# Optimization experiments

Measured on AMD Instinct MI355X. Metric: run time of the kernel, lower is better.

The kernel has to match this reference:

```python
import jax, jax.numpy as jnp
import numpy as np

N_NODES = 100000

def setup_inputs() -> dict:
    key = jax.random.key(0)
    k1, k2, k3, k4 = jax.random.split(key, 4)
    feat = jax.random.normal(k1, (N_NODES, 128), dtype=jnp.float32)
    weight = jax.random.normal(k2, (128, 64), dtype=jnp.float32) * 0.05
    src = jax.random.randint(k3, (600000,), 0, N_NODES, dtype=jnp.int64)
    dst = jax.random.randint(k4, (600000,), 0, N_NODES, dtype=jnp.int64)
    return {"feat": feat, "weight": weight, "src": src, "dst": dst}

def reference(feat, weight, src, dst):
    n = feat.shape[0]
    ones = jnp.ones(src.shape[0], dtype=jnp.float32)
    # out-degree of source nodes (edges leave src), in-degree of dst nodes
    out_deg = jnp.clip(jax.ops.segment_sum(ones, src, num_segments=n), 1.0)
    in_deg = jnp.clip(jax.ops.segment_sum(ones, dst, num_segments=n), 1.0)
    norm_src = (out_deg ** -0.5)[:, None]   # [N,1]
    norm_dst = (in_deg ** -0.5)[:, None]    # [N,1]
    # in_feats (128) > out_feats (64): project first, then aggregate
    h = jnp.matmul(feat, weight) * norm_src              # [N, 64]
    msgs = h[src]                                        # [E, 64] gather
    rst = jax.ops.segment_sum(msgs, dst, num_segments=n)  # [N, 64] scatter-sum
    rst = rst * norm_dst
    return rst
```

## Files before the change

kernel.cpp:

```cpp
#include <hip/hip_runtime.h>
#include <hip/hip_fp16.h>

#define IN_F 128
#define OUT_F 64
#define NB    256
#define BSH   9
#define CAP   3840
#define CHUNK 2048
#define KPF  136
#define KPW  144

using short8  = __attribute__((ext_vector_type(8))) short;
using float4v = __attribute__((ext_vector_type(4))) float;

static __device__ inline unsigned short f2bf(float x) {
    union { float f; unsigned u; } v; v.f = x;
    unsigned r = (v.u + 0x7fffu + ((v.u >> 16) & 1u)) >> 16;
    return (unsigned short)r;
}

__global__ __launch_bounds__(256) void bin_kernel(
    const int* __restrict__ src, const int* __restrict__ dst,
    int* __restrict__ gcur_d, int* __restrict__ gcur_s,
    unsigned* __restrict__ bkt_d, unsigned short* __restrict__ bkt_s, int E)
{
    __shared__ int hd[NB], hs[NB], based[NB], bases[NB];
    const int tid = threadIdx.x;
    const int e0  = blockIdx.x * CHUNK;

    hd[tid] = 0; hs[tid] = 0;
    __syncthreads();

    int sv[8], dv[8];
    #pragma unroll
    for (int j = 0; j < 8; ++j) {
        int i = e0 + j * 256 + tid;
        if (i < E) { sv[j] = src[i]; dv[j] = dst[i]; }
        else       { sv[j] = -1;     dv[j] = -1; }
    }
    #pragma unroll
    for (int j = 0; j < 8; ++j) {
        if (dv[j] >= 0) {
            atomicAdd(&hd[dv[j] >> BSH], 1);
            atomicAdd(&hs[sv[j] >> BSH], 1);
        }
    }
    __syncthreads();

    int cd = hd[tid], cs = hs[tid];
    based[tid] = cd ? atomicAdd(&gcur_d[tid], cd) : 0;
    bases[tid] = cs ? atomicAdd(&gcur_s[tid], cs) : 0;
    hd[tid] = 0; hs[tid] = 0;
    __syncthreads();

    #pragma unroll
    for (int j = 0; j < 8; ++j) {
        if (dv[j] >= 0) {
            int bd = dv[j] >> BSH;
            int pd = atomicAdd(&hd[bd], 1) + based[bd];
            if (pd < CAP)
                bkt_d[(size_t)bd * CAP + pd] =
                    (unsigned)sv[j] | ((unsigned)(dv[j] & 511) << 17);
            int bs = sv[j] >> BSH;
            int ps = atomicAdd(&hs[bs], 1) + bases[bs];
            if (ps < CAP) bkt_s[(size_t)bs * CAP + ps] = (unsigned short)(sv[j] & 511);
        }
    }
}

__global__ __launch_bounds__(256) void csr_kernel(
    const unsigned* __restrict__ bkt_d, const unsigned short* __restrict__ bkt_s,
    const int* __restrict__ gcur_d, const int* __restrict__ gcur_s,
    int2* __restrict__ off_deg, int* __restrict__ ebuf, int* __restrict__ outdeg, int n)
{
    __shared__ int hist[512], curs[512], hist_s[512], sc[256];
    const int b = blockIdx.x, tid = threadIdx.x;
    const int cnt   = min(gcur_d[b], CAP);
    const int cnt_s = min(gcur_s[b], CAP);

    hist[tid] = 0; hist[tid + 256] = 0;
    hist_s[tid] = 0; hist_s[tid + 256] = 0;
    __syncthreads();

    unsigned rec[15];
    int nrec = 0;
    for (int i = tid; i < cnt; i += 256) {
        unsigned e = bkt_d[(size_t)b * CAP + i];
        rec[nrec++] = e;
        atomicAdd(&hist[e >> 17], 1);
    }
    for (int i = tid; i < cnt_s; i += 256)
        atomicAdd(&hist_s[bkt_s[(size_t)b * CAP + i]], 1);
    __syncthreads();

    int a0 = hist[2 * tid], a1 = hist[2 * tid + 1];
    int psum = a0 + a1;
    sc[tid] = psum; __syncthreads();
    for (int o = 1; o < 256; o <<= 1) {
        int t = (tid >= o) ? sc[tid - o] : 0;
        __syncthreads();
        sc[tid] += t;
        __syncthreads();
    }
    int excl = sc[tid] - psum;
    curs[2 * tid]     = excl;
    curs[2 * tid + 1] = excl + a0;
    off_deg[b * 512 + 2 * tid]     = make_int2(b * CAP + excl,      a0);
    off_deg[b * 512 + 2 * tid + 1] = make_int2(b * CAP + excl + a0, a1);
    __syncthreads();

    for (int j = 0; j < nrec; ++j) {
        unsigned e = rec[j];
        int p = atomicAdd(&curs[e >> 17], 1);
        if (p < CAP) ebuf[b * CAP + p] = (int)(e & 0x1FFFFu);
    }

    int node = b * 512 + tid;
    if (node < n) outdeg[node] = hist_s[tid];
    node += 256;
    if (node < n) outdeg[node] = hist_s[tid + 256];
}

__global__ __launch_bounds__(256) void gemm_norm_kernel(
    const float* __restrict__ feat,
    const float* __restrict__ W,
    const int*   __restrict__ outdeg,
    __half* __restrict__ h,
    int n)
{
    __shared__ unsigned short Fh[128 * KPF];
    __shared__ unsigned short Wt[64 * KPW];

    const int tid  = threadIdx.x;
    const int row0 = blockIdx.x * 128;

    {
        const float4* W4 = (const float4*)W;
        #pragma unroll
        for (int it = 0; it < 8; ++it) {
            int i4 = it * 256 + tid;
            int k  = i4 >> 4;
            int c4 = (i4 & 15) * 4;
            float4 wv = W4[i4];
            Wt[(c4 + 0) * KPW + k] = f2bf(wv.x);
            Wt[(c4 + 1) * KPW + k] = f2bf(wv.y);
            Wt[(c4 + 2) * KPW + k] = f2bf(wv.z);
            Wt[(c4 + 3) * KPW + k] = f2bf(wv.w);
        }
    }
    {
        const float4* F4 = (const float4*)feat;
        #pragma unroll
        for (int it = 0; it < 16; ++it) {
            int i4 = it * 256 + tid;
            int r  = i4 >> 5;
            int c4 = (i4 & 31) * 4;
            int gr = row0 + r; if (gr >= n) gr = n - 1;
            float4 v = F4[(long)gr * 32 + (i4 & 31)];
            ushort4 u;
            u.x = f2bf(v.x); u.y = f2bf(v.y); u.z = f2bf(v.z); u.w = f2bf(v.w);
            *(ushort4*)&Fh[r * KPF + c4] = u;
        }
    }
    __syncthreads();

    const int w  = tid >> 6;
    const int l  = tid & 63;
    const int ml = l & 15;
    const int q  = l >> 4;

    float4v acc[2][4];
    #pragma unroll
    for (int rt = 0; rt < 2; ++rt)
        #pragma unroll
        for (int ct = 0; ct < 4; ++ct)
            acc[rt][ct] = (float4v){0.f, 0.f, 0.f, 0.f};

    #pragma unroll
    for (int ks = 0; ks < 4; ++ks) {
        const int ko = ks * 32 + q * 8;
        short8 a0 = *(const short8*)&Fh[(w * 32 +  0 + ml) * KPF + ko];
        short8 a1 = *(const short8*)&Fh[(w * 32 + 16 + ml) * KPF + ko];
        short8 b0 = *(const short8*)&Wt[( 0 + ml) * KPW + ko];
        short8 b1 = *(const short8*)&Wt[(16 + ml) * KPW + ko];
        short8 b2 = *(const short8*)&Wt[(32 + ml) * KPW + ko];
        short8 b3 = *(const short8*)&Wt[(48 + ml) * KPW + ko];
        acc[0][0] = __builtin_amdgcn_mfma_f32_16x16x32_bf16(a0, b0, acc[0][0], 0, 0, 0);
        acc[0][1] = __builtin_amdgcn_mfma_f32_16x16x32_bf16(a0, b1, acc[0][1], 0, 0, 0);
        acc[0][2] = __builtin_amdgcn_mfma_f32_16x16x32_bf16(a0, b2, acc[0][2], 0, 0, 0);
        acc[0][3] = __builtin_amdgcn_mfma_f32_16x16x32_bf16(a0, b3, acc[0][3], 0, 0, 0);
        acc[1][0] = __builtin_amdgcn_mfma_f32_16x16x32_bf16(a1, b0, acc[1][0], 0, 0, 0);
        acc[1][1] = __builtin_amdgcn_mfma_f32_16x16x32_bf16(a1, b1, acc[1][1], 0, 0, 0);
        acc[1][2] = __builtin_amdgcn_mfma_f32_16x16x32_bf16(a1, b2, acc[1][2], 0, 0, 0);
        acc[1][3] = __builtin_amdgcn_mfma_f32_16x16x32_bf16(a1, b3, acc[1][3], 0, 0, 0);
    }

    #pragma unroll
    for (int rt = 0; rt < 2; ++rt) {
        #pragma unroll
        for (int reg = 0; reg < 4; ++reg) {
            int row = row0 + w * 32 + rt * 16 + q * 4 + reg;
            if (row < n) {
                float ns = rsqrtf(fmaxf((float)outdeg[row], 1.0f));
                #pragma unroll
                for (int ct = 0; ct < 4; ++ct)
                    h[(long)row * OUT_F + ct * 16 + ml] = __float2half(acc[rt][ct][reg] * ns);
            }
        }
    }
}

__global__ __launch_bounds__(256) void gather_kernel(
    const int* __restrict__ ebuf, const int2* __restrict__ off_deg,
    const __half* __restrict__ h, float* __restrict__ out, int n)
{
    int d = blockIdx.x * 4 + (threadIdx.x >> 6);
    int l = threadIdx.x & 63;
    int o = l >> 3;
    int t = l & 7;
    if (d >= n) return;
    int2 od = off_deg[d];
    int beg = od.x, m = od.y, end = od.x + od.y;
    float a0 = 0.f, a1 = 0.f, a2 = 0.f, a3 = 0.f;
    float a4 = 0.f, a5 = 0.f, a6 = 0.f, a7 = 0.f;
    for (int j = beg + o; j < end; j += 8) {
        int s = ebuf[j];
        union { uint4 u; __half2 h2[4]; } P;
        P.u = *(const uint4*)&h[(long)s * OUT_F + 8 * t];
        float2 f0 = __half22float2(P.h2[0]);
        float2 f1 = __half22float2(P.h2[1]);
        float2 f2 = __half22float2(P.h2[2]);
        float2 f3 = __half22float2(P.h2[3]);
        a0 += f0.x; a1 += f0.y; a2 += f1.x; a3 += f1.y;
        a4 += f2.x; a5 += f2.y; a6 += f3.x; a7 += f3.y;
    }
    #pragma unroll
    for (int mask = 8; mask <= 32; mask <<= 1) {
        a0 += __shfl_xor(a0, mask); a1 += __shfl_xor(a1, mask);
        a2 += __shfl_xor(a2, mask); a3 += __shfl_xor(a3, mask);
        a4 += __shfl_xor(a4, mask); a5 += __shfl_xor(a5, mask);
        a6 += __shfl_xor(a6, mask); a7 += __shfl_xor(a7, mask);
    }
    if (o == 0) {
        float nd = rsqrtf(fmaxf((float)m, 1.0f));
        float4 v0 = make_float4(a0 * nd, a1 * nd, a2 * nd, a3 * nd);
        float4 v1 = make_float4(a4 * nd, a5 * nd, a6 * nd, a7 * nd);
        *(float4*)&out[(long)d * OUT_F + 8 * t]     = v0;
        *(float4*)&out[(long)d * OUT_F + 8 * t + 4] = v1;
    }
}

extern "C" void kernel_launch(void* const* d_in, const int* in_sizes, int n_in,
                              void* d_out, int out_size, void* d_ws, size_t ws_size,
                              hipStream_t stream) {
    const float* feat = (const float*)d_in[0];
    const float* W    = (const float*)d_in[1];
    const int*   src  = (const int*)d_in[2];
    const int*   dst  = (const int*)d_in[3];
    float* out = (float*)d_out;

    const int n = in_sizes[0] / IN_F;
    const int E = in_sizes[2];

    char* wsb = (char*)d_ws;
    int* gcur_d = (int*)wsb;
    int* gcur_s = gcur_d + NB;
    int* outdeg = gcur_s + NB;
    size_t pos = (((size_t)(2 * NB + n)) * 4 + 15) & ~(size_t)15;
    int2* off_deg = (int2*)(wsb + pos);
    pos = (pos + (size_t)NB * 512 * 8 + 15) & ~(size_t)15;
    int* ebuf = (int*)(wsb + pos);
    pos = (pos + (size_t)NB * CAP * 4 + 15) & ~(size_t)15;
    unsigned* bkt_d = (unsigned*)(wsb + pos);
    pos = (pos + (size_t)NB * CAP * 4 + 15) & ~(size_t)15;
    unsigned short* bkt_s = (unsigned short*)(wsb + pos);
    pos = (pos + (size_t)NB * CAP * 2 + 15) & ~(size_t)15;
    __half* h = (__half*)(wsb + pos);

    hipMemsetAsync(gcur_d, 0, 2 * NB * sizeof(int), stream);

    bin_kernel<<<(E + CHUNK - 1) / CHUNK, 256, 0, stream>>>(src, dst, gcur_d, gcur_s,
                                                            bkt_d, bkt_s, E);
    csr_kernel<<<NB, 256, 0, stream>>>(bkt_d, bkt_s, gcur_d, gcur_s,
                                       off_deg, ebuf, outdeg, n);
    gemm_norm_kernel<<<(n + 127) / 128, 256, 0, stream>>>(feat, W, outdeg, h, n);
    gather_kernel<<<(n + 3) / 4, 256, 0, stream>>>(ebuf, off_deg, h, out, n);
}
```

Measured before the change: 158.4 us.

## Compute out-degree with global atomics instead of source-node bucketing

Out-degree is now counted with direct global atomicAdd per edge into a zeroed outdeg array, which removes the source-bucket pass (bkt_s writes, the second shared histogram and its readback in csr_kernel). The CSR block scan switches from a barrier-heavy shared-memory scan to wavefront shuffle scans combined through per-wave sums. Edges are reread from global memory in the scatter pass instead of being held in registers. The cost is 600k scattered global atomics and a larger memset covering n ints.

```diff
diff --git a/kernel.cpp b/kernel.cpp
--- a/kernel.cpp
+++ b/kernel.cpp
@@ -21,14 +21,14 @@
 
 __global__ __launch_bounds__(256) void bin_kernel(
     const int* __restrict__ src, const int* __restrict__ dst,
-    int* __restrict__ gcur_d, int* __restrict__ gcur_s,
-    unsigned* __restrict__ bkt_d, unsigned short* __restrict__ bkt_s, int E)
-{
-    __shared__ int hd[NB], hs[NB], based[NB], bases[NB];
+    int* __restrict__ gcur_d, int* __restrict__ outdeg,
+    unsigned* __restrict__ bkt_d, int E)
+{
+    __shared__ int hd[NB], based[NB];
     const int tid = threadIdx.x;
     const int e0  = blockIdx.x * CHUNK;
 
-    hd[tid] = 0; hs[tid] = 0;
+    hd[tid] = 0;
     __syncthreads();
 
     int sv[8], dv[8];
@@ -42,15 +42,14 @@
     for (int j = 0; j < 8; ++j) {
         if (dv[j] >= 0) {
             atomicAdd(&hd[dv[j] >> BSH], 1);
-            atomicAdd(&hs[sv[j] >> BSH], 1);
-        }
-    }
-    __syncthreads();
-
-    int cd = hd[tid], cs = hs[tid];
+            atomicAdd(&outdeg[sv[j]], 1);
+        }
+    }
+    __syncthreads();
+
+    int cd = hd[tid];
     based[tid] = cd ? atomicAdd(&gcur_d[tid], cd) : 0;
-    bases[tid] = cs ? atomicAdd(&gcur_s[tid], cs) : 0;
-    hd[tid] = 0; hs[tid] = 0;
+    hd[tid] = 0;
     __syncthreads();
 
     #pragma unroll
@@ -61,64 +60,52 @@
             if (pd < CAP)
                 bkt_d[(size_t)bd * CAP + pd] =
                     (unsigned)sv[j] | ((unsigned)(dv[j] & 511) << 17);
-            int bs = sv[j] >> BSH;
-            int ps = atomicAdd(&hs[bs], 1) + bases[bs];
-            if (ps < CAP) bkt_s[(size_t)bs * CAP + ps] = (unsigned short)(sv[j] & 511);
         }
     }
 }
 
 __global__ __launch_bounds__(256) void csr_kernel(
-    const unsigned* __restrict__ bkt_d, const unsigned short* __restrict__ bkt_s,
-    const int* __restrict__ gcur_d, const int* __restrict__ gcur_s,
-    int2* __restrict__ off_deg, int* __restrict__ ebuf, int* __restrict__ outdeg, int n)
-{
-    __shared__ int hist[512], curs[512], hist_s[512], sc[256];
+    const unsigned* __restrict__ bkt_d, const int* __restrict__ gcur_d,
+    int2* __restrict__ off_deg, int* __restrict__ ebuf)
+{
+    __shared__ int hist[512], curs[512];
+    __shared__ int wsum[4];
     const int b = blockIdx.x, tid = threadIdx.x;
-    const int cnt   = min(gcur_d[b], CAP);
-    const int cnt_s = min(gcur_s[b], CAP);
+    const int cnt = min(gcur_d[b], CAP);
 
     hist[tid] = 0; hist[tid + 256] = 0;
-    hist_s[tid] = 0; hist_s[tid + 256] = 0;
-    __syncthreads();
-
-    unsigned rec[15];
-    int nrec = 0;
-    for (int i = tid; i < cnt; i += 256) {
-        unsigned e = bkt_d[(size_t)b * CAP + i];
-        rec[nrec++] = e;
-        atomicAdd(&hist[e >> 17], 1);
-    }
-    for (int i = tid; i < cnt_s; i += 256)
-        atomicAdd(&hist_s[bkt_s[(size_t)b * CAP + i]], 1);
+    __syncthreads();
+
+    const unsigned* bp = bkt_d + (size_t)b * CAP;
+    for (int i = tid; i < cnt; i += 256)
+        atomicAdd(&hist[bp[i] >> 17], 1);
     __syncthreads();
 
     int a0 = hist[2 * tid], a1 = hist[2 * tid + 1];
     int psum = a0 + a1;
-    sc[tid] = psum; __syncthreads();
-    for (int o = 1; o < 256; o <<= 1) {
-        int t = (tid >= o) ? sc[tid - o] : 0;
-        __syncthreads();
-        sc[tid] += t;
-        __syncthreads();
-    }
-    int excl = sc[tid] - psum;
+    const int lane = tid & 63, w = tid >> 6;
+    int x = psum;
+    #pragma unroll
+    for (int off = 1; off < 64; off <<= 1) {
+        int y = __shfl_up(x, off);
+        if (lane >= off) x += y;
+    }
+    if (lane == 63) wsum[w] = x;
+    __syncthreads();
+    int wbase = 0;
+    for (int i = 0; i < w; ++i) wbase += wsum[i];
+    int excl = x + wbase - psum;
     curs[2 * tid]     = excl;
     curs[2 * tid + 1] = excl + a0;
     off_deg[b * 512 + 2 * tid]     = make_int2(b * CAP + excl,      a0);
     off_deg[b * 512 + 2 * tid + 1] = make_int2(b * CAP + excl + a0, a1);
     __syncthreads();
 
-    for (int j = 0; j < nrec; ++j) {
-        unsigned e = rec[j];
+    for (int i = tid; i < cnt; i += 256) {
+        unsigned e = bp[i];
         int p = atomicAdd(&curs[e >> 17], 1);
         if (p < CAP) ebuf[b * CAP + p] = (int)(e & 0x1FFFFu);
     }
-
-    int node = b * 512 + tid;
-    if (node < n) outdeg[node] = hist_s[tid];
-    node += 256;
-    if (node < n) outdeg[node] = hist_s[tid + 256];
 }
 
 __global__ __launch_bounds__(256) void gemm_norm_kernel(
@@ -264,25 +251,21 @@
 
     char* wsb = (char*)d_ws;
     int* gcur_d = (int*)wsb;
-    int* gcur_s = gcur_d + NB;
-    int* outdeg = gcur_s + NB;
-    size_t pos = (((size_t)(2 * NB + n)) * 4 + 15) & ~(size_t)15;
+    int* outdeg = gcur_d + NB;
+    size_t pos = (((size_t)(NB + n)) * 4 + 15) & ~(size_t)15;
     int2* off_deg = (int2*)(wsb + pos);
     pos = (pos + (size_t)NB * 512 * 8 + 15) & ~(size_t)15;
     int* ebuf = (int*)(wsb + pos);
     pos = (pos + (size_t)NB * CAP * 4 + 15) & ~(size_t)15;
     unsigned* bkt_d = (unsigned*)(wsb + pos);
     pos = (pos + (size_t)NB * CAP * 4 + 15) & ~(size_t)15;
-    unsigned short* bkt_s = (unsigned short*)(wsb + pos);
-    pos = (pos + (size_t)NB * CAP * 2 + 15) & ~(size_t)15;
     __half* h = (__half*)(wsb + pos);
 
-    hipMemsetAsync(gcur_d, 0, 2 * NB * sizeof(int), stream);
-
-    bin_kernel<<<(E + CHUNK - 1) / CHUNK, 256, 0, stream>>>(src, dst, gcur_d, gcur_s,
-                                                            bkt_d, bkt_s, E);
-    csr_kernel<<<NB, 256, 0, stream>>>(bkt_d, bkt_s, gcur_d, gcur_s,
-                                       off_deg, ebuf, outdeg, n);
+    hipMemsetAsync(gcur_d, 0, (NB + n) * sizeof(int), stream);
+
+    bin_kernel<<<(E + CHUNK - 1) / CHUNK, 256, 0, stream>>>(src, dst, gcur_d, outdeg,
+                                                            bkt_d, E);
+    csr_kernel<<<NB, 256, 0, stream>>>(bkt_d, gcur_d, off_deg, ebuf);
     gemm_norm_kernel<<<(n + 127) / 128, 256, 0, stream>>>(feat, W, outdeg, h, n);
     gather_kernel<<<(n + 3) / 4, 256, 0, stream>>>(ebuf, off_deg, h, out, n);
 }
```

After: 174.9 us. +10.4%, slower.

## Fuse edge binning with GEMM in one launch and apply source norm in gather

Applied to the files above, without the earlier changes.

Binning blocks and GEMM blocks now share one kernel launch, using a shared-memory union, so the edge binning and the dense projection run concurrently. The source-degree normalization moves out of the GEMM epilogue into the gather loop, which reads outdeg per edge and uses an FMA; this removes the GEMM's dependence on the CSR pass. The CSR kernel's block scan is replaced with a wavefront shuffle scan plus per-wave sums. The trade-off is an extra outdeg gather and rsqrt per edge in the gather kernel, plus the larger shared-memory footprint of the fused kernel.

```diff
diff --git a/kernel.cpp b/kernel.cpp
--- a/kernel.cpp
+++ b/kernel.cpp
@@ -19,120 +19,68 @@
     return (unsigned short)r;
 }
 
-__global__ __launch_bounds__(256) void bin_kernel(
+__global__ __launch_bounds__(256) void bin_gemm_kernel(
     const int* __restrict__ src, const int* __restrict__ dst,
     int* __restrict__ gcur_d, int* __restrict__ gcur_s,
-    unsigned* __restrict__ bkt_d, unsigned short* __restrict__ bkt_s, int E)
+    unsigned* __restrict__ bkt_d, unsigned short* __restrict__ bkt_s,
+    int E, int nbin,
+    const float* __restrict__ feat, const float* __restrict__ W,
+    __half* __restrict__ h, int n)
 {
-    __shared__ int hd[NB], hs[NB], based[NB], bases[NB];
+    __shared__ union {
+        struct { int hd[NB]; int hs[NB]; int based[NB]; int bases[NB]; } bin;
+        struct { unsigned short Fh[128 * KPF]; unsigned short Wt[64 * KPW]; } gm;
+    } smem;
+
     const int tid = threadIdx.x;
-    const int e0  = blockIdx.x * CHUNK;
-
-    hd[tid] = 0; hs[tid] = 0;
-    __syncthreads();
-
-    int sv[8], dv[8];
-    #pragma unroll
-    for (int j = 0; j < 8; ++j) {
-        int i = e0 + j * 256 + tid;
-        if (i < E) { sv[j] = src[i]; dv[j] = dst[i]; }
-        else       { sv[j] = -1;     dv[j] = -1; }
-    }
-    #pragma unroll
-    for (int j = 0; j < 8; ++j) {
-        if (dv[j] >= 0) {
-            atomicAdd(&hd[dv[j] >> BSH], 1);
-            atomicAdd(&hs[sv[j] >> BSH], 1);
-        }
-    }
-    __syncthreads();
-
-    int cd = hd[tid], cs = hs[tid];
-    based[tid] = cd ? atomicAdd(&gcur_d[tid], cd) : 0;
-    bases[tid] = cs ? atomicAdd(&gcur_s[tid], cs) : 0;
-    hd[tid] = 0; hs[tid] = 0;
-    __syncthreads();
-
-    #pragma unroll
-    for (int j = 0; j < 8; ++j) {
-        if (dv[j] >= 0) {
-            int bd = dv[j] >> BSH;
-            int pd = atomicAdd(&hd[bd], 1) + based[bd];
-            if (pd < CAP)
-                bkt_d[(size_t)bd * CAP + pd] =
-                    (unsigned)sv[j] | ((unsigned)(dv[j] & 511) << 17);
-            int bs = sv[j] >> BSH;
-            int ps = atomicAdd(&hs[bs], 1) + bases[bs];
-            if (ps < CAP) bkt_s[(size_t)bs * CAP + ps] = (unsigned short)(sv[j] & 511);
-        }
-    }
-}
-
-__global__ __launch_bounds__(256) void csr_kernel(
-    const unsigned* __restrict__ bkt_d, const unsigned short* __restrict__ bkt_s,
-    const int* __restrict__ gcur_d, const int* __restrict__ gcur_s,
-    int2* __restrict__ off_deg, int* __restrict__ ebuf, int* __restrict__ outdeg, int n)
-{
-    __shared__ int hist[512], curs[512], hist_s[512], sc[256];
-    const int b = blockIdx.x, tid = threadIdx.x;
-    const int cnt   = min(gcur_d[b], CAP);
-    const int cnt_s = min(gcur_s[b], CAP);
-
-    hist[tid] = 0; hist[tid + 256] = 0;
-    hist_s[tid] = 0; hist_s[tid + 256] = 0;
-    __syncthreads();
-
-    unsigned rec[15];
-    int nrec = 0;
-    for (int i = tid; i < cnt; i += 256) {
-        unsigned e = bkt_d[(size_t)b * CAP + i];
-        rec[nrec++] = e;
-        atomicAdd(&hist[e >> 17], 1);
-    }
-    for (int i = tid; i < cnt_s; i += 256)
-        atomicAdd(&hist_s[bkt_s[(size_t)b * CAP + i]], 1);
-    __syncthreads();
-
-    int a0 = hist[2 * tid], a1 = hist[2 * tid + 1];
-    int psum = a0 + a1;
-    sc[tid] = psum; __syncthreads();
-    for (int o = 1; o < 256; o <<= 1) {
-        int t = (tid >= o) ? sc[tid - o] : 0;
+
+    if (blockIdx.x < (unsigned)nbin) {
+        const int e0 = blockIdx.x * CHUNK;
+
+        smem.bin.hd[tid] = 0; smem.bin.hs[tid] = 0;
         __syncthreads();
-        sc[tid] += t;
+
+        int sv[8], dv[8];
+        #pragma unroll
+        for (int j = 0; j < 8; ++j) {
+            int i = e0 + j * 256 + tid;
+            if (i < E) { sv[j] = src[i]; dv[j] = dst[i]; }
+            else       { sv[j] = -1;     dv[j] = -1; }
+        }
+        #pragma unroll
+        for (int j = 0; j < 8; ++j) {
+            if (dv[j] >= 0) {
+                atomicAdd(&smem.bin.hd[dv[j] >> BSH], 1);
+                atomicAdd(&smem.bin.hs[sv[j] >> BSH], 1);
+            }
+        }
         __syncthreads();
-    }
-    int excl = sc[tid] - psum;
-    curs[2 * tid]     = excl;
-    curs[2 * tid + 1] = excl + a0;
-    off_deg[b * 512 + 2 * tid]     = make_int2(b * CAP + excl,      a0);
-    off_deg[b * 512 + 2 * tid + 1] = make_int2(b * CAP + excl + a0, a1);
-    __syncthreads();
-
-    for (int j = 0; j < nrec; ++j) {
-        unsigned e = rec[j];
-        int p = atomicAdd(&curs[e >> 17], 1);
-        if (p < CAP) ebuf[b * CAP + p] = (int)(e & 0x1FFFFu);
-    }
-
-    int node = b * 512 + tid;
-    if (node < n) outdeg[node] = hist_s[tid];
-    node += 256;
-    if (node < n) outdeg[node] = hist_s[tid + 256];
-}
-
-__global__ __launch_bounds__(256) void gemm_norm_kernel(
-    const float* __restrict__ feat,
-    const float* __restrict__ W,
-    const int*   __restrict__ outdeg,
-    __half* __restrict__ h,
-    int n)
-{
-    __shared__ unsigned short Fh[128 * KPF];
-    __shared__ unsigned short Wt[64 * KPW];
-
-    const int tid  = threadIdx.x;
-    const int row0 = blockIdx.x * 128;
+
+        int cd = smem.bin.hd[tid], cs = smem.bin.hs[tid];
+        smem.bin.based[tid] = cd ? atomicAdd(&gcur_d[tid], cd) : 0;
+        smem.bin.bases[tid] = cs ? atomicAdd(&gcur_s[tid], cs) : 0;
+        smem.bin.hd[tid] = 0; smem.bin.hs[tid] = 0;
+        __syncthreads();
+
+        #pragma unroll
+        for (int j = 0; j < 8; ++j) {
+            if (dv[j] >= 0) {
+                int bd = dv[j] >> BSH;
+                int pd = atomicAdd(&smem.bin.hd[bd], 1) + smem.bin.based[bd];
+                if (pd < CAP)
+                    bkt_d[(size_t)bd * CAP + pd] =
+                        (unsigned)sv[j] | ((unsigned)(dv[j] & 511) << 17);
+                int bs = sv[j] >> BSH;
+                int ps = atomicAdd(&smem.bin.hs[bs], 1) + smem.bin.bases[bs];
+                if (ps < CAP) bkt_s[(size_t)bs * CAP + ps] = (unsigned short)(sv[j] & 511);
+            }
+        }
+        return;
+    }
+
+    unsigned short* Fh = smem.gm.Fh;
+    unsigned short* Wt = smem.gm.Wt;
+    const int row0 = (blockIdx.x - nbin) * 128;
 
     {
         const float4* W4 = (const float4*)W;
@@ -201,17 +149,75 @@
         for (int reg = 0; reg < 4; ++reg) {
             int row = row0 + w * 32 + rt * 16 + q * 4 + reg;
             if (row < n) {
-                float ns = rsqrtf(fmaxf((float)outdeg[row], 1.0f));
                 #pragma unroll
                 for (int ct = 0; ct < 4; ++ct)
-                    h[(long)row * OUT_F + ct * 16 + ml] = __float2half(acc[rt][ct][reg] * ns);
+                    h[(long)row * OUT_F + ct * 16 + ml] = __float2half(acc[rt][ct][reg]);
             }
         }
     }
+}
+
+__global__ __launch_bounds__(256) void csr_kernel(
+    const unsigned* __restrict__ bkt_d, const unsigned short* __restrict__ bkt_s,
+    const int* __restrict__ gcur_d, const int* __restrict__ gcur_s,
+    int2* __restrict__ off_deg, int* __restrict__ ebuf, int* __restrict__ outdeg, int n)
+{
+    __shared__ int hist[512], curs[512], hist_s[512];
+    __shared__ int wsum[4];
+    const int b = blockIdx.x, tid = threadIdx.x;
+    const int cnt   = min(gcur_d[b], CAP);
+    const int cnt_s = min(gcur_s[b], CAP);
+
+    hist[tid] = 0; hist[tid + 256] = 0;
+    hist_s[tid] = 0; hist_s[tid + 256] = 0;
+    __syncthreads();
+
+    unsigned rec[15];
+    int nrec = 0;
+    for (int i = tid; i < cnt; i += 256) {
+        unsigned e = bkt_d[(size_t)b * CAP + i];
+        rec[nrec++] = e;
+        atomicAdd(&hist[e >> 17], 1);
+    }
+    for (int i = tid; i < cnt_s; i += 256)
+        atomicAdd(&hist_s[bkt_s[(size_t)b * CAP + i]], 1);
+    __syncthreads();
+
+    int a0 = hist[2 * tid], a1 = hist[2 * tid + 1];
+    int psum = a0 + a1;
+    const int lane = tid & 63, w = tid >> 6;
+    int x = psum;
+    #pragma unroll
+    for (int off = 1; off < 64; off <<= 1) {
+        int y = __shfl_up(x, off);
+        if (lane >= off) x += y;
+    }
+    if (lane == 63) wsum[w] = x;
+    __syncthreads();
+    int wbase = 0;
+    for (int i = 0; i < w; ++i) wbase += wsum[i];
+    int excl = x + wbase - psum;
+    curs[2 * tid]     = excl;
+    curs[2 * tid + 1] = excl + a0;
+    off_deg[b * 512 + 2 * tid]     = make_int2(b * CAP + excl,      a0);
+    off_deg[b * 512 + 2 * tid + 1] = make_int2(b * CAP + excl + a0, a1);
+    __syncthreads();
+
+    for (int j = 0; j < nrec; ++j) {
+        unsigned e = rec[j];
+        int p = atomicAdd(&curs[e >> 17], 1);
+        if (p < CAP) ebuf[b * CAP + p] = (int)(e & 0x1FFFFu);
+    }
+
+    int node = b * 512 + tid;
+    if (node < n) outdeg[node] = hist_s[tid];
+    node += 256;
+    if (node < n) outdeg[node] = hist_s[tid + 256];
 }
 
 __global__ __launch_bounds__(256) void gather_kernel(
     const int* __restrict__ ebuf, const int2* __restrict__ off_deg,
+    const int* __restrict__ outdeg,
     const __half* __restrict__ h, float* __restrict__ out, int n)
 {
     int d = blockIdx.x * 4 + (threadIdx.x >> 6);
@@ -225,14 +231,17 @@
     float a4 = 0.f, a5 = 0.f, a6 = 0.f, a7 = 0.f;
     for (int j = beg + o; j < end; j += 8) {
         int s = ebuf[j];
+        float ns = rsqrtf(fmaxf((float)outdeg[s], 1.0f));
         union { uint4 u; __half2 h2[4]; } P;
         P.u = *(const uint4*)&h[(long)s * OUT_F + 8 * t];
         float2 f0 = __half22float2(P.h2[0]);
         float2 f1 = __half22float2(P.h2[1]);
         float2 f2 = __half22float2(P.h2[2]);
         float2 f3 = __half22float2(P.h2[3]);
-        a0 += f0.x; a1 += f0.y; a2 += f1.x; a3 += f1.y;
-        a4 += f2.x; a5 += f2.y; a6 += f3.x; a7 += f3.y;
+        a0 = fmaf(f0.x, ns, a0); a1 = fmaf(f0.y, ns, a1);
+        a2 = fmaf(f1.x, ns, a2); a3 = fmaf(f1.y, ns, a3);
+        a4 = fmaf(f2.x, ns, a4); a5 = fmaf(f2.y, ns, a5);
+        a6 = fmaf(f3.x, ns, a6); a7 = fmaf(f3.y, ns, a7);
     }
     #pragma unroll
     for (int mask = 8; mask <= 32; mask <<= 1) {
@@ -279,10 +288,13 @@
 
     hipMemsetAsync(gcur_d, 0, 2 * NB * sizeof(int), stream);
 
-    bin_kernel<<<(E + CHUNK - 1) / CHUNK, 256, 0, stream>>>(src, dst, gcur_d, gcur_s,
-                                                            bkt_d, bkt_s, E);
+    const int nbin  = (E + CHUNK - 1) / CHUNK;
+    const int ngemm = (n + 127) / 128;
+
+    bin_gemm_kernel<<<nbin + ngemm, 256, 0, stream>>>(src, dst, gcur_d, gcur_s,
+                                                      bkt_d, bkt_s, E, nbin,
+                                                      feat, W, h, n);
     csr_kernel<<<NB, 256, 0, stream>>>(bkt_d, bkt_s, gcur_d, gcur_s,
                                        off_deg, ebuf, outdeg, n);
-    gemm_norm_kernel<<<(n + 127) / 128, 256, 0, stream>>>(feat, W, outdeg, h, n);
-    gather_kernel<<<(n + 3) / 4, 256, 0, stream>>>(ebuf, off_deg, h, out, n);
-}
+    gather_kernel<<<(n + 3) / 4, 256, 0, stream>>>(ebuf, off_deg, outdeg, h, out, n);
+}
```

Result: no change. 155.9 us (-1.6%).
